# Performance work log

Hardware: AMD Instinct MI355X
Metric: run time of the kernel (lower is better)

## Reference

```python
import jax, jax.numpy as jnp
import numpy as np

B, N, D_OBS, D_MSG, H = 4096, 64, 128, 64, 4
HD = D_MSG // H
EPS = 1e-5


def setup_inputs() -> dict:
    key = jax.random.key(0)
    ks = jax.random.split(key, 16)
    def w(k, shape):
        fan_in = shape[0]
        return (jax.random.normal(k, shape, dtype=jnp.float32) / np.sqrt(fan_in)).astype(jnp.float32)
    return {
        'obs_all': jax.random.normal(ks[0], (B, N, D_OBS), dtype=jnp.float32),
        # msg encoder: Linear(obs,128) -> ReLU -> Linear(128,msg)
        'enc_w1': w(ks[1], (D_OBS, 128)), 'enc_b1': jnp.zeros((128,), jnp.float32),
        'enc_w2': w(ks[2], (128, D_MSG)), 'enc_b2': jnp.zeros((D_MSG,), jnp.float32),
        # MultiheadAttention in/out projections (stored as (in, out))
        'in_proj_w': w(ks[3], (D_MSG, 3 * D_MSG)), 'in_proj_b': jnp.zeros((3 * D_MSG,), jnp.float32),
        'out_w': w(ks[4], (D_MSG, D_MSG)), 'out_b': jnp.zeros((D_MSG,), jnp.float32),
        # integrator: Linear(obs+msg,256) -> LayerNorm(256) -> ReLU -> Linear(256,obs)
        'int_w1': w(ks[5], (D_OBS + D_MSG, 256)), 'int_b1': jnp.zeros((256,), jnp.float32),
        'ln_g': jnp.ones((256,), jnp.float32), 'ln_b': jnp.zeros((256,), jnp.float32),
        'int_w2': w(ks[6], (256, D_OBS)), 'int_b2': jnp.zeros((D_OBS,), jnp.float32),
    }


def reference(obs_all, enc_w1, enc_b1, enc_w2, enc_b2,
              in_proj_w, in_proj_b, out_w, out_b,
              int_w1, int_b1, ln_g, ln_b, int_w2, int_b2):
    # --- send: encode observations into messages (B, N, msg_dim) ---
    h = jax.nn.relu(obs_all @ enc_w1 + enc_b1)
    msgs = h @ enc_w2 + enc_b2

    # --- attention aggregation: per-agent query over all messages.
    # The original per-agent loop (query = msgs[:, i:i+1]) is exactly
    # batched self-attention over the agent axis.
    qkv = msgs @ in_proj_w + in_proj_b            # (B, N, 3*msg)
    q, k, v = jnp.split(qkv, 3, axis=-1)
    q = q.reshape(B, N, H, HD)
    k = k.reshape(B, N, H, HD)
    v = v.reshape(B, N, H, HD)
    scale = 1.0 / np.sqrt(HD)
    scores = jnp.einsum('bqhd,bkhd->bhqk', q, k) * scale   # (B, H, N, N)
    attn = jax.nn.softmax(scores, axis=-1)
    ctx = jnp.einsum('bhqk,bkhd->bqhd', attn, v).reshape(B, N, D_MSG)
    agg = ctx @ out_w + out_b                     # (B, N, msg_dim)

    # --- receive: concat obs + aggregated message, MLP with LayerNorm ---
    combined = jnp.concatenate([obs_all, agg], axis=-1)
    z = combined @ int_w1 + int_b1                # (B, N, 256)
    mu = jnp.mean(z, axis=-1, keepdims=True)
    var = jnp.var(z, axis=-1, keepdims=True)
    z = (z - mu) * jax.lax.rsqrt(var + EPS) * ln_g + ln_b
    enriched = jax.nn.relu(z) @ int_w2 + int_b2   # (B, N, obs_dim)
    return enriched, msgs
```

## Files before the change

### kernel.cpp

```cpp
#include <hip/hip_runtime.h>


typedef __attribute__((ext_vector_type(8))) short bf16x8;
typedef __attribute__((ext_vector_type(4))) float f32x4;
typedef __attribute__((ext_vector_type(16))) float f32x16;

#define MFMA16(a, b, c) __builtin_amdgcn_mfma_f32_16x16x32_bf16((a), (b), (c), 0, 0, 0)
#define MFMA32(a, b, c) __builtin_amdgcn_mfma_f32_32x32x16_bf16((a), (b), (c), 0, 0, 0)

__device__ __forceinline__ float b2f(short s) {
    union { unsigned u; float f; } x;
    x.u = ((unsigned)(unsigned short)s) << 16;
    return x.f;
}
__device__ __forceinline__ short f2b(float f) {
    union { float f; unsigned u; } x;
    x.f = f;
    unsigned r = (x.u + 0x7FFFu + ((x.u >> 16) & 1u)) >> 16;
    return (short)r;
}

template<bool F32>
__device__ __forceinline__ float ldS(const void* p, int i) {
    if (F32) return ((const float*)p)[i];
    return b2f(((const short*)p)[i]);
}
template<bool F32>
__device__ __forceinline__ bf16x8 ld8(const void* p, long i) {
    if (F32) {
        const float4* f = (const float4*)((const float*)p + i);
        float4 a = f[0], b = f[1];
        bf16x8 r;
        r[0] = f2b(a.x); r[1] = f2b(a.y); r[2] = f2b(a.z); r[3] = f2b(a.w);
        r[4] = f2b(b.x); r[5] = f2b(b.y); r[6] = f2b(b.z); r[7] = f2b(b.w);
        return r;
    }
    return *(const bf16x8*)((const short*)p + i);
}
template<bool F32, bool OBSBF>
__device__ __forceinline__ bf16x8 ldobs(const void* obs, const short* obs_bf, long i) {
    if (OBSBF) return *(const bf16x8*)(obs_bf + i);
    return ld8<F32>(obs, i);
}
template<bool F32>
__device__ __forceinline__ void st(void* p, long i, float v) {
    if (F32) ((float*)p)[i] = v;
    else ((short*)p)[i] = f2b(v);
}

#define P_S   0
#define H_S   0
#define Z_S   0
#define Q2_S  9216
#define AG_S  9216
#define K2_S  13312
#define VT_S  17408
#define LN_S  17408
#define MU_S  18432
#define MS_S  22016
#define SMEM_SHORTS 26624
#define HP 136
#define MP 72
#define ZP 264
#define PP 72
#define VP 72

#define WT1_OFF   0
#define WT2_OFF   16384
#define WTQ_OFF   24576
#define WTO_OFF   36864
#define WTI1_OFF  40960
#define WTI2_OFF  90112
#define WT_TOTAL  122880
#define OBS_ELEMS 33554432L
#define WS_NEEDED (256UL + (unsigned long)WT_TOTAL * 2 + (unsigned long)OBS_ELEMS * 2)

template<bool DO_CONV>
__global__ void prep(const void* __restrict__ obs,
                     const void* __restrict__ w1, const void* __restrict__ w2,
                     const void* __restrict__ wq, const void* __restrict__ wo,
                     const void* __restrict__ wi1, const void* __restrict__ wi2,
                     int* __restrict__ flag, short* __restrict__ wt,
                     short* __restrict__ obs_bf) {
    const unsigned short* o16 = (const unsigned short*)obs;
    int lane = threadIdx.x & 63;
    int cnt = 0;
    for (int i = lane; i < 512; i += 64) {
        unsigned e = (o16[i] >> 7) & 0xFFu;
        cnt += (e == 0u || (e >= 80u && e <= 140u)) ? 1 : 0;
    }
#pragma unroll
    for (int off = 1; off < 64; off <<= 1) cnt += __shfl_xor(cnt, off);
    const bool isbf16 = (cnt >= 480);
    if (blockIdx.x == 0 && threadIdx.x == 0) *flag = isbf16 ? 1 : 0;

    long id = (long)blockIdx.x * 256 + threadIdx.x;
    if (id < WT_TOTAL) {
        const void* src;
        int K, N, off, loc = (int)id;
        if (loc < 16384)      { src = w1;  K = 128; N = 128; off = WT1_OFF; }
        else if (loc < 24576) { src = w2;  K = 128; N = 64;  off = WT2_OFF;  loc -= 16384; }
        else if (loc < 36864) { src = wq;  K = 64;  N = 192; off = WTQ_OFF;  loc -= 24576; }
        else if (loc < 40960) { src = wo;  K = 64;  N = 64;  off = WTO_OFF;  loc -= 36864; }
        else if (loc < 90112) { src = wi1; K = 192; N = 256; off = WTI1_OFF; loc -= 40960; }
        else                  { src = wi2; K = 256; N = 128; off = WTI2_OFF; loc -= 90112; }
        int n = loc / K;
        int k = loc - n * K;
        float v = isbf16 ? b2f(((const short*)src)[k * N + n]) : ((const float*)src)[k * N + n];
        wt[off + loc] = f2b(v);
    } else if (DO_CONV && !isbf16) {
        long base = (id - WT_TOTAL) * 8;
        if (base < OBS_ELEMS) {
            const float4* f = (const float4*)((const float*)obs + base);
            float4 a = f[0], b = f[1];
            bf16x8 r;
            r[0] = f2b(a.x); r[1] = f2b(a.y); r[2] = f2b(a.z); r[3] = f2b(a.w);
            r[4] = f2b(b.x); r[5] = f2b(b.y); r[6] = f2b(b.z); r[7] = f2b(b.w);
            *(bf16x8*)(obs_bf + base) = r;
        }
    }
}

template<bool F32, bool OBSBF>
__global__ __launch_bounds__(256, 3)
void macs_main(const void* __restrict__ obs,
               const void* __restrict__ eb1, const void* __restrict__ eb2,
               const void* __restrict__ ipb, const void* __restrict__ ob,
               const void* __restrict__ ib1, const void* __restrict__ lg,
               const void* __restrict__ lb,  const void* __restrict__ ib2,
               const int* __restrict__ flag, const short* __restrict__ wt,
               const short* __restrict__ obs_bf, void* __restrict__ out) {
    if (*flag != (F32 ? 0 : 1)) return;
    __shared__ __align__(16) short smem[SMEM_SHORTS];
    const int tid = threadIdx.x;
    const int w = tid >> 6;
    const int lane = tid & 63;
    const int q = lane >> 4;
    const int t = lane & 15;
    const int l31 = lane & 31;
    const int hi = lane >> 5;
    const int b = blockIdx.x;
    const long obase = (long)b * 64 * 128;

    {
        bf16x8 oa[4][4];
#pragma unroll
        for (int ks = 0; ks < 4; ++ks)
#pragma unroll
            for (int mt = 0; mt < 4; ++mt)
                oa[ks][mt] = ldobs<F32, OBSBF>(obs, obs_bf, obase + (mt * 16 + t) * 128 + ks * 32 + q * 8);
        f32x4 acc[4][2] = {};
        const short* wt1 = wt + WT1_OFF;
#pragma unroll
        for (int ks = 0; ks < 4; ++ks) {
            bf16x8 bb[2];
#pragma unroll
            for (int tj = 0; tj < 2; ++tj)
                bb[tj] = *(const bf16x8*)(wt1 + (w * 32 + tj * 16 + t) * 128 + ks * 32 + q * 8);
#pragma unroll
            for (int mt = 0; mt < 4; ++mt)
#pragma unroll
                for (int tj = 0; tj < 2; ++tj)
                    acc[mt][tj] = MFMA16(oa[ks][mt], bb[tj], acc[mt][tj]);
        }
        short* hs = smem + H_S;
#pragma unroll
        for (int tj = 0; tj < 2; ++tj) {
            int c = w * 32 + tj * 16 + t;
            float bias = ldS<F32>(eb1, c);
#pragma unroll
            for (int mt = 0; mt < 4; ++mt)
#pragma unroll
                for (int i = 0; i < 4; ++i) {
                    int r = mt * 16 + q * 4 + i;
                    hs[r * HP + c] = f2b(fmaxf(acc[mt][tj][i] + bias, 0.f));
                }
        }
    }
    __syncthreads();

    {
        bf16x8 bbv[4];
        const short* wt2 = wt + WT2_OFF;
#pragma unroll
        for (int ks = 0; ks < 4; ++ks)
            bbv[ks] = *(const bf16x8*)(wt2 + (w * 16 + t) * 128 + ks * 32 + q * 8);
        f32x4 acc[4] = {};
        const short* hs = smem + H_S;
#pragma unroll
        for (int ks = 0; ks < 4; ++ks) {
            bf16x8 a[4];
#pragma unroll
            for (int mt = 0; mt < 4; ++mt)
                a[mt] = *(const bf16x8*)(hs + (mt * 16 + t) * HP + ks * 32 + q * 8);
#pragma unroll
            for (int mt = 0; mt < 4; ++mt)
                acc[mt] = MFMA16(a[mt], bbv[ks], acc[mt]);
        }
        short* ms = smem + MS_S;
        float bias = ldS<F32>(eb2, w * 16 + t);
        const long msgs_base = 33554432L;
#pragma unroll
        for (int mt = 0; mt < 4; ++mt)
#pragma unroll
            for (int i = 0; i < 4; ++i) {
                int r = mt * 16 + q * 4 + i;
                float v = acc[mt][i] + bias;
                ms[r * MP + w * 16 + t] = f2b(v);
                st<F32>(out, msgs_base + ((long)b * 64 + r) * 64 + w * 16 + t, v);
            }
    }
    __syncthreads();

    {
        bf16x8 bbv[6];
        const short* wtq = wt + WTQ_OFF;
#pragma unroll
        for (int ks = 0; ks < 2; ++ks)
#pragma unroll
            for (int tj = 0; tj < 3; ++tj)
                bbv[ks * 3 + tj] = *(const bf16x8*)(wtq + (w * 48 + tj * 16 + t) * 64 + ks * 32 + q * 8);
        f32x4 acc[4][3] = {};
        const short* ms = smem + MS_S;
#pragma unroll
        for (int ks = 0; ks < 2; ++ks) {
            bf16x8 a[4];
#pragma unroll
            for (int mt = 0; mt < 4; ++mt)
                a[mt] = *(const bf16x8*)(ms + (mt * 16 + t) * MP + ks * 32 + q * 8);
#pragma unroll
            for (int mt = 0; mt < 4; ++mt)
#pragma unroll
                for (int tj = 0; tj < 3; ++tj)
                    acc[mt][tj] = MFMA16(a[mt], bbv[ks * 3 + tj], acc[mt][tj]);
        }
#pragma unroll
        for (int tj = 0; tj < 3; ++tj) {
            int c = w * 48 + tj * 16 + t;
            float bias = ldS<F32>(ipb, c);
            int sec = c >> 6;
            int head = (c >> 4) & 3;
            float scale = (sec == 0) ? 0.25f : 1.0f;
#pragma unroll
            for (int mt = 0; mt < 4; ++mt)
#pragma unroll
                for (int i = 0; i < 4; ++i) {
                    int r = mt * 16 + q * 4 + i;
                    short bv = f2b((acc[mt][tj][i] + bias) * scale);
                    int idx;
                    if (sec == 0)      idx = Q2_S + head * 1024 + r * 16 + t;
                    else if (sec == 1) idx = K2_S + head * 1024 + r * 16 + t;
                    else               idx = VT_S + head * 1152 + t * VP + r;
                    smem[idx] = bv;
                }
        }
    }
    __syncthreads();

    {
        const int rh = w & 1;
        short* Pq = smem + P_S + w * 2304;
        short* cs = smem + MS_S;
#pragma unroll
        for (int p = 0; p < 2; ++p) {
            const int hd = p * 2 + (w >> 1);
            const short* qh = smem + Q2_S + hd * 1024;
            const short* kh = smem + K2_S + hd * 1024;
            const short* vh = smem + VT_S + hd * 1152;
            f32x16 sc0 = {}, sc1 = {};
            {
                bf16x8 aq  = *(const bf16x8*)(qh + (rh * 32 + l31) * 16 + hi * 8);
                bf16x8 bk0 = *(const bf16x8*)(kh + l31 * 16 + hi * 8);
                bf16x8 bk1 = *(const bf16x8*)(kh + (32 + l31) * 16 + hi * 8);
                sc0 = MFMA32(aq, bk0, sc0);
                sc1 = MFMA32(aq, bk1, sc1);
            }
#pragma unroll
            for (int i = 0; i < 16; ++i) {
                int lr = (i & 3) + 8 * (i >> 2) + 4 * hi;
                float e0 = __expf(sc0[i]);
                float e1 = __expf(sc1[i]);
                float s = e0 + e1;
#pragma unroll
                for (int off = 1; off < 32; off <<= 1) s += __shfl_xor(s, off);
                float inv = 1.f / s;
                Pq[lr * PP + l31]      = f2b(e0 * inv);
                Pq[lr * PP + 32 + l31] = f2b(e1 * inv);
            }
            f32x4 cx[2] = {};
#pragma unroll
            for (int ks = 0; ks < 2; ++ks) {
                bf16x8 bb = *(const bf16x8*)(vh + t * VP + ks * 32 + q * 8);
                bf16x8 a0 = *(const bf16x8*)(Pq + t * PP + ks * 32 + q * 8);
                bf16x8 a1 = *(const bf16x8*)(Pq + (16 + t) * PP + ks * 32 + q * 8);
                cx[0] = MFMA16(a0, bb, cx[0]);
                cx[1] = MFMA16(a1, bb, cx[1]);
            }
#pragma unroll
            for (int mt = 0; mt < 2; ++mt)
#pragma unroll
                for (int i = 0; i < 4; ++i)
                    cs[(rh * 32 + mt * 16 + q * 4 + i) * MP + hd * 16 + t] = f2b(cx[mt][i]);
        }
    }
    __syncthreads();

    bf16x8 oa6[4][4];
    {
#pragma unroll
        for (int ks = 0; ks < 4; ++ks)
#pragma unroll
            for (int mt = 0; mt < 4; ++mt)
                oa6[ks][mt] = ldobs<F32, OBSBF>(obs, obs_bf, obase + (mt * 16 + t) * 128 + ks * 32 + q * 8);
        bf16x8 bbv[2];
        const short* wto = wt + WTO_OFF;
#pragma unroll
        for (int ks = 0; ks < 2; ++ks)
            bbv[ks] = *(const bf16x8*)(wto + (w * 16 + t) * 64 + ks * 32 + q * 8);
        f32x4 acc[4] = {};
        const short* cs = smem + MS_S;
#pragma unroll
        for (int ks = 0; ks < 2; ++ks) {
            bf16x8 a[4];
#pragma unroll
            for (int mt = 0; mt < 4; ++mt)
                a[mt] = *(const bf16x8*)(cs + (mt * 16 + t) * MP + ks * 32 + q * 8);
#pragma unroll
            for (int mt = 0; mt < 4; ++mt)
                acc[mt] = MFMA16(a[mt], bbv[ks], acc[mt]);
        }
        short* ag = smem + AG_S;
        float bias = ldS<F32>(ob, w * 16 + t);
#pragma unroll
        for (int mt = 0; mt < 4; ++mt)
#pragma unroll
            for (int i = 0; i < 4; ++i)
                ag[(mt * 16 + q * 4 + i) * MP + w * 16 + t] = f2b(acc[mt][i] + bias);
    }
    __syncthreads();

    {
        f32x4 acc[4][4] = {};
        const short* wti1 = wt + WTI1_OFF;
        const short* ag = smem + AG_S;
#pragma unroll
        for (int ks = 0; ks < 6; ++ks) {
            bf16x8 a[4], bb[4];
            if (ks < 4) {
#pragma unroll
                for (int mt = 0; mt < 4; ++mt)
                    a[mt] = oa6[ks][mt];
            } else {
#pragma unroll
                for (int mt = 0; mt < 4; ++mt)
                    a[mt] = *(const bf16x8*)(ag + (mt * 16 + t) * MP + (ks - 4) * 32 + q * 8);
            }
#pragma unroll
            for (int tj = 0; tj < 4; ++tj)
                bb[tj] = *(const bf16x8*)(wti1 + (w * 64 + tj * 16 + t) * 192 + ks * 32 + q * 8);
#pragma unroll
            for (int mt = 0; mt < 4; ++mt)
#pragma unroll
                for (int tj = 0; tj < 4; ++tj)
                    acc[mt][tj] = MFMA16(a[mt], bb[tj], acc[mt][tj]);
        }
#pragma unroll
        for (int tj = 0; tj < 4; ++tj) {
            float bias = ldS<F32>(ib1, w * 64 + tj * 16 + t);
#pragma unroll
            for (int mt = 0; mt < 4; ++mt)
#pragma unroll
                for (int i = 0; i < 4; ++i) acc[mt][tj][i] += bias;
        }
        float2* lnred = (float2*)(smem + LN_S);
#pragma unroll
        for (int mt = 0; mt < 4; ++mt)
#pragma unroll
            for (int i = 0; i < 4; ++i) {
                float s = 0.f, s2 = 0.f;
#pragma unroll
                for (int tj = 0; tj < 4; ++tj) {
                    float v = acc[mt][tj][i];
                    s += v;
                    s2 += v * v;
                }
#pragma unroll
                for (int off = 1; off < 16; off <<= 1) {
                    s += __shfl_xor(s, off);
                    s2 += __shfl_xor(s2, off);
                }
                if (t == 0) {
                    float2 p; p.x = s; p.y = s2;
                    lnred[(mt * 16 + q * 4 + i) * 4 + w] = p;
                }
            }
        __syncthreads();
        float2* munr = (float2*)(smem + MU_S);
        if (tid < 64) {
            float S = 0.f, S2 = 0.f;
#pragma unroll
            for (int j = 0; j < 4; ++j) {
                float2 p = lnred[tid * 4 + j];
                S += p.x;
                S2 += p.y;
            }
            float mu = S * (1.f / 256.f);
            float var = S2 * (1.f / 256.f) - mu * mu;
            float2 m; m.x = mu; m.y = rsqrtf(fmaxf(var, 0.f) + 1e-5f);
            munr[tid] = m;
        }
        __syncthreads();
        short* zs = smem + Z_S;
        float gv[4], bv[4];
#pragma unroll
        for (int tj = 0; tj < 4; ++tj) {
            gv[tj] = ldS<F32>(lg, w * 64 + tj * 16 + t);
            bv[tj] = ldS<F32>(lb, w * 64 + tj * 16 + t);
        }
#pragma unroll
        for (int mt = 0; mt < 4; ++mt)
#pragma unroll
            for (int i = 0; i < 4; ++i) {
                int r = mt * 16 + q * 4 + i;
                float2 mr = munr[r];
#pragma unroll
                for (int tj = 0; tj < 4; ++tj) {
                    float v = (acc[mt][tj][i] - mr.x) * mr.y * gv[tj] + bv[tj];
                    zs[r * ZP + w * 64 + tj * 16 + t] = f2b(fmaxf(v, 0.f));
                }
            }
    }
    __syncthreads();

    {
        bf16x8 bbv[8][2];
        const short* wti2 = wt + WTI2_OFF;
#pragma unroll
        for (int ks = 0; ks < 8; ++ks)
#pragma unroll
            for (int tj = 0; tj < 2; ++tj)
                bbv[ks][tj] = *(const bf16x8*)(wti2 + (w * 32 + tj * 16 + t) * 256 + ks * 32 + q * 8);
        f32x4 acc[4][2] = {};
        const short* zs = smem + Z_S;
#pragma unroll
        for (int ks = 0; ks < 8; ++ks) {
            bf16x8 a[4];
#pragma unroll
            for (int mt = 0; mt < 4; ++mt)
                a[mt] = *(const bf16x8*)(zs + (mt * 16 + t) * ZP + ks * 32 + q * 8);
#pragma unroll
            for (int mt = 0; mt < 4; ++mt)
#pragma unroll
                for (int tj = 0; tj < 2; ++tj)
                    acc[mt][tj] = MFMA16(a[mt], bbv[ks][tj], acc[mt][tj]);
        }
#pragma unroll
        for (int tj = 0; tj < 2; ++tj) {
            int c = w * 32 + tj * 16 + t;
            float bias = ldS<F32>(ib2, c);
#pragma unroll
            for (int mt = 0; mt < 4; ++mt)
#pragma unroll
                for (int i = 0; i < 4; ++i) {
                    int r = mt * 16 + q * 4 + i;
                    st<F32>(out, ((long)b * 64 + r) * 128 + c, acc[mt][tj][i] + bias);
                }
        }
    }
}

extern "C" void kernel_launch(void* const* d_in, const int* in_sizes, int n_in,
                              void* d_out, int out_size, void* d_ws, size_t ws_size,
                              hipStream_t stream) {
    const void* obs = d_in[0];
    const void* w1  = d_in[1];
    const void* b1  = d_in[2];
    const void* w2  = d_in[3];
    const void* b2  = d_in[4];
    const void* wq  = d_in[5];
    const void* bq  = d_in[6];
    const void* wo  = d_in[7];
    const void* bo  = d_in[8];
    const void* wi1 = d_in[9];
    const void* bi1 = d_in[10];
    const void* lg  = d_in[11];
    const void* lb  = d_in[12];
    const void* wi2 = d_in[13];
    const void* bi2 = d_in[14];
    int* flag = (int*)d_ws;
    short* wt = (short*)d_ws + 128;
    short* obs_bf = (short*)d_ws + 128 + WT_TOTAL;
    const bool big_ws = (ws_size >= WS_NEEDED);

    if (big_ws) {
        prep<true><<<dim3(16864), dim3(256), 0, stream>>>(obs, w1, w2, wq, wo, wi1, wi2, flag, wt, obs_bf);
        macs_main<false, false><<<dim3(4096), dim3(256), 0, stream>>>(obs, b1, b2, bq, bo, bi1, lg, lb, bi2, flag, wt, obs_bf, d_out);
        macs_main<true,  true ><<<dim3(4096), dim3(256), 0, stream>>>(obs, b1, b2, bq, bo, bi1, lg, lb, bi2, flag, wt, obs_bf, d_out);
    } else {
        prep<false><<<dim3(480), dim3(256), 0, stream>>>(obs, w1, w2, wq, wo, wi1, wi2, flag, wt, obs_bf);
        macs_main<false, false><<<dim3(4096), dim3(256), 0, stream>>>(obs, b1, b2, bq, bo, bi1, lg, lb, bi2, flag, wt, obs_bf, d_out);
        macs_main<true,  false><<<dim3(4096), dim3(256), 0, stream>>>(obs, b1, b2, bq, bo, bi1, lg, lb, bi2, flag, wt, obs_bf, d_out);
    }
}
```

Baseline: 586.7 us.

## Fold linear layers into prep weights, defer softmax normalization, single main launch

Precomputes fused weights in prep: enc_w2·in_proj (QKV straight from the hidden layer) and out_w·int_w1 (context straight into the integrator), with matching folded biases and all bias/LN vectors converted to fp32. The main kernel skips the msgs→QKV and agg stages and their shared-memory round trips. Softmax normalization now comes from an extra MFMA against a ones vector and is applied after P·V, which removes the per-row shuffle reductions. It also prefetches later-stage weights into registers, reuses the first obs fragment load, and replaces the two dtype-templated launches with one runtime-branched launch. The folded weights are rounded to bf16, which changes numerics, and the larger register footprint may reduce occupancy.

Result: no change. 586.9 us (+0.0%).

```diff
diff --git a/kernel.cpp b/kernel.cpp
--- a/kernel.cpp
+++ b/kernel.cpp
@@ -19,45 +19,28 @@
     unsigned r = (x.u + 0x7FFFu + ((x.u >> 16) & 1u)) >> 16;
     return (short)r;
 }
-
-template<bool F32>
-__device__ __forceinline__ float ldS(const void* p, int i) {
-    if (F32) return ((const float*)p)[i];
-    return b2f(((const short*)p)[i]);
-}
-template<bool F32>
-__device__ __forceinline__ bf16x8 ld8(const void* p, long i) {
-    if (F32) {
-        const float4* f = (const float4*)((const float*)p + i);
-        float4 a = f[0], b = f[1];
-        bf16x8 r;
-        r[0] = f2b(a.x); r[1] = f2b(a.y); r[2] = f2b(a.z); r[3] = f2b(a.w);
-        r[4] = f2b(b.x); r[5] = f2b(b.y); r[6] = f2b(b.z); r[7] = f2b(b.w);
-        return r;
-    }
-    return *(const bf16x8*)((const short*)p + i);
-}
-template<bool F32, bool OBSBF>
-__device__ __forceinline__ bf16x8 ldobs(const void* obs, const short* obs_bf, long i) {
-    if (OBSBF) return *(const bf16x8*)(obs_bf + i);
-    return ld8<F32>(obs, i);
-}
-template<bool F32>
-__device__ __forceinline__ void st(void* p, long i, float v) {
-    if (F32) ((float*)p)[i] = v;
-    else ((short*)p)[i] = f2b(v);
+__device__ __forceinline__ float ldw(const void* p, long i, bool bf) {
+    return bf ? b2f(((const short*)p)[i]) : ((const float*)p)[i];
+}
+__device__ __forceinline__ bf16x8 ld8rt(const void* p, long i, bool bf) {
+    if (bf) return *(const bf16x8*)((const short*)p + i);
+    const float4* f = (const float4*)((const float*)p + i);
+    float4 a = f[0], c = f[1];
+    bf16x8 r;
+    r[0] = f2b(a.x); r[1] = f2b(a.y); r[2] = f2b(a.z); r[3] = f2b(a.w);
+    r[4] = f2b(c.x); r[5] = f2b(c.y); r[6] = f2b(c.z); r[7] = f2b(c.w);
+    return r;
 }
 
 #define P_S   0
 #define H_S   0
 #define Z_S   0
 #define Q2_S  9216
-#define AG_S  9216
 #define K2_S  13312
 #define VT_S  17408
 #define LN_S  17408
 #define MU_S  18432
-#define MS_S  22016
+#define CTX_S 22016
 #define SMEM_SHORTS 26624
 #define HP 136
 #define MP 72
@@ -67,21 +50,33 @@
 
 #define WT1_OFF   0
 #define WT2_OFF   16384
-#define WTQ_OFF   24576
-#define WTO_OFF   36864
-#define WTI1_OFF  40960
-#define WTI2_OFF  90112
-#define WT_TOTAL  122880
+#define WT26_OFF  24576
+#define WTI1_OFF  49152
+#define WTF_OFF   81920
+#define WTI2_OFF  98304
+#define WT_TOTAL  131072
+#define FB_B26 0
+#define FB_BI  192
+#define FB_EB1 448
+#define FB_EB2 576
+#define FB_LG  640
+#define FB_LB  896
+#define FB_IB2 1152
+#define FB_TOTAL 1280
 #define OBS_ELEMS 33554432L
-#define WS_NEEDED (256UL + (unsigned long)WT_TOTAL * 2 + (unsigned long)OBS_ELEMS * 2)
+#define WS_NEEDED ((unsigned long)(128 + WT_TOTAL + 2 * FB_TOTAL + OBS_ELEMS) * 2UL)
 
 template<bool DO_CONV>
 __global__ void prep(const void* __restrict__ obs,
                      const void* __restrict__ w1, const void* __restrict__ w2,
                      const void* __restrict__ wq, const void* __restrict__ wo,
                      const void* __restrict__ wi1, const void* __restrict__ wi2,
+                     const void* __restrict__ eb1, const void* __restrict__ eb2,
+                     const void* __restrict__ ipb, const void* __restrict__ ob,
+                     const void* __restrict__ ib1, const void* __restrict__ lg,
+                     const void* __restrict__ lb,  const void* __restrict__ ib2,
                      int* __restrict__ flag, short* __restrict__ wt,
-                     short* __restrict__ obs_bf) {
+                     float* __restrict__ fb, short* __restrict__ obs_bf) {
     const unsigned short* o16 = (const unsigned short*)obs;
     int lane = threadIdx.x & 63;
     int cnt = 0;
@@ -91,46 +86,69 @@
     }
 #pragma unroll
     for (int off = 1; off < 64; off <<= 1) cnt += __shfl_xor(cnt, off);
-    const bool isbf16 = (cnt >= 480);
-    if (blockIdx.x == 0 && threadIdx.x == 0) *flag = isbf16 ? 1 : 0;
+    const bool bf = (cnt >= 480);
+    if (blockIdx.x == 0 && threadIdx.x == 0) *flag = bf ? 1 : 0;
 
     long id = (long)blockIdx.x * 256 + threadIdx.x;
-    if (id < WT_TOTAL) {
-        const void* src;
-        int K, N, off, loc = (int)id;
-        if (loc < 16384)      { src = w1;  K = 128; N = 128; off = WT1_OFF; }
-        else if (loc < 24576) { src = w2;  K = 128; N = 64;  off = WT2_OFF;  loc -= 16384; }
-        else if (loc < 36864) { src = wq;  K = 64;  N = 192; off = WTQ_OFF;  loc -= 24576; }
-        else if (loc < 40960) { src = wo;  K = 64;  N = 64;  off = WTO_OFF;  loc -= 36864; }
-        else if (loc < 90112) { src = wi1; K = 192; N = 256; off = WTI1_OFF; loc -= 40960; }
-        else                  { src = wi2; K = 256; N = 128; off = WTI2_OFF; loc -= 90112; }
-        int n = loc / K;
-        int k = loc - n * K;
-        float v = isbf16 ? b2f(((const short*)src)[k * N + n]) : ((const float*)src)[k * N + n];
-        wt[off + loc] = f2b(v);
-    } else if (DO_CONV && !isbf16) {
-        long base = (id - WT_TOTAL) * 8;
+    if (id < 16384) {
+        int n = (int)id >> 7, k = (int)id & 127;
+        wt[WT1_OFF + id] = f2b(ldw(w1, k * 128 + n, bf));
+    } else if (id < 24576) {
+        int loc = (int)id - 16384, n = loc >> 7, k = loc & 127;
+        wt[WT2_OFF + loc] = f2b(ldw(w2, k * 64 + n, bf));
+    } else if (id < 49152) {
+        int loc = (int)id - 24576, n = loc >> 7, k = loc & 127;
+        float s = 0.f;
+        for (int j = 0; j < 64; ++j) s += ldw(w2, k * 64 + j, bf) * ldw(wq, j * 192 + n, bf);
+        wt[WT26_OFF + loc] = f2b(s);
+    } else if (id < 81920) {
+        int loc = (int)id - 49152, n = loc >> 7, k = loc & 127;
+        wt[WTI1_OFF + loc] = f2b(ldw(wi1, k * 256 + n, bf));
+    } else if (id < 98304) {
+        int loc = (int)id - 81920, n = loc >> 6, c = loc & 63;
+        float s = 0.f;
+        for (int m = 0; m < 64; ++m) s += ldw(wo, c * 64 + m, bf) * ldw(wi1, (128 + m) * 256 + n, bf);
+        wt[WTF_OFF + loc] = f2b(s);
+    } else if (id < 131072) {
+        int loc = (int)id - 98304, n = loc >> 8, k = loc & 255;
+        wt[WTI2_OFF + loc] = f2b(ldw(wi2, k * 128 + n, bf));
+    } else if (id < 131264) {
+        int n = (int)id - 131072;
+        float s = ldw(ipb, n, bf);
+        for (int j = 0; j < 64; ++j) s += ldw(eb2, j, bf) * ldw(wq, j * 192 + n, bf);
+        fb[FB_B26 + n] = s;
+    } else if (id < 131520) {
+        int n = (int)id - 131264;
+        float s = ldw(ib1, n, bf);
+        for (int m = 0; m < 64; ++m) s += ldw(ob, m, bf) * ldw(wi1, (128 + m) * 256 + n, bf);
+        fb[FB_BI + n] = s;
+    } else if (id < 132352) {
+        int j = (int)id - 131520;
+        float v; int d;
+        if (j < 128)      { v = ldw(eb1, j, bf);       d = FB_EB1 + j; }
+        else if (j < 192) { v = ldw(eb2, j - 128, bf); d = FB_EB2 + j - 128; }
+        else if (j < 448) { v = ldw(lg, j - 192, bf);  d = FB_LG + j - 192; }
+        else if (j < 704) { v = ldw(lb, j - 448, bf);  d = FB_LB + j - 448; }
+        else              { v = ldw(ib2, j - 704, bf); d = FB_IB2 + j - 704; }
+        fb[d] = v;
+    } else if (DO_CONV && !bf) {
+        long base = (id - 132352) * 8;
         if (base < OBS_ELEMS) {
             const float4* f = (const float4*)((const float*)obs + base);
-            float4 a = f[0], b = f[1];
+            float4 a = f[0], c = f[1];
             bf16x8 r;
             r[0] = f2b(a.x); r[1] = f2b(a.y); r[2] = f2b(a.z); r[3] = f2b(a.w);
-            r[4] = f2b(b.x); r[5] = f2b(b.y); r[6] = f2b(b.z); r[7] = f2b(b.w);
+            r[4] = f2b(c.x); r[5] = f2b(c.y); r[6] = f2b(c.z); r[7] = f2b(c.w);
             *(bf16x8*)(obs_bf + base) = r;
         }
     }
 }
 
-template<bool F32, bool OBSBF>
+template<bool OBSBF>
 __global__ __launch_bounds__(256, 3)
-void macs_main(const void* __restrict__ obs,
-               const void* __restrict__ eb1, const void* __restrict__ eb2,
-               const void* __restrict__ ipb, const void* __restrict__ ob,
-               const void* __restrict__ ib1, const void* __restrict__ lg,
-               const void* __restrict__ lb,  const void* __restrict__ ib2,
-               const int* __restrict__ flag, const short* __restrict__ wt,
+void macs_main(const void* __restrict__ obs, const int* __restrict__ flag,
+               const short* __restrict__ wt, const float* __restrict__ fb,
                const short* __restrict__ obs_bf, void* __restrict__ out) {
-    if (*flag != (F32 ? 0 : 1)) return;
     __shared__ __align__(16) short smem[SMEM_SHORTS];
     const int tid = threadIdx.x;
     const int w = tid >> 6;
@@ -141,52 +159,63 @@
     const int hi = lane >> 5;
     const int b = blockIdx.x;
     const long obase = (long)b * 64 * 128;
+    const bool inbf = (*flag != 0);
+    const bool f32out = !inbf;
+    const short* osrc = OBSBF ? (inbf ? (const short*)obs : obs_bf) : (const short*)0;
+
+    bf16x8 oa[4][4];
+#pragma unroll
+    for (int ks = 0; ks < 4; ++ks)
+#pragma unroll
+        for (int mt = 0; mt < 4; ++mt) {
+            long idx = obase + (mt * 16 + t) * 128 + ks * 32 + q * 8;
+            oa[ks][mt] = OBSBF ? *(const bf16x8*)(osrc + idx) : ld8rt(obs, idx, inbf);
+        }
+
+    bf16x8 w2p[4];
+    bf16x8 wi1p[2][4];
+    bf16x8 w2pp[8][2];
 
     {
-        bf16x8 oa[4][4];
-#pragma unroll
-        for (int ks = 0; ks < 4; ++ks)
-#pragma unroll
-            for (int mt = 0; mt < 4; ++mt)
-                oa[ks][mt] = ldobs<F32, OBSBF>(obs, obs_bf, obase + (mt * 16 + t) * 128 + ks * 32 + q * 8);
         f32x4 acc[4][2] = {};
-        const short* wt1 = wt + WT1_OFF;
+        const short* wt1p = wt + WT1_OFF;
 #pragma unroll
         for (int ks = 0; ks < 4; ++ks) {
             bf16x8 bb[2];
 #pragma unroll
             for (int tj = 0; tj < 2; ++tj)
-                bb[tj] = *(const bf16x8*)(wt1 + (w * 32 + tj * 16 + t) * 128 + ks * 32 + q * 8);
+                bb[tj] = *(const bf16x8*)(wt1p + (w * 32 + tj * 16 + t) * 128 + ks * 32 + q * 8);
 #pragma unroll
             for (int mt = 0; mt < 4; ++mt)
 #pragma unroll
                 for (int tj = 0; tj < 2; ++tj)
                     acc[mt][tj] = MFMA16(oa[ks][mt], bb[tj], acc[mt][tj]);
         }
+        {
+            const short* wt2 = wt + WT2_OFF;
+#pragma unroll
+            for (int ks = 0; ks < 4; ++ks)
+                w2p[ks] = *(const bf16x8*)(wt2 + (w * 16 + t) * 128 + ks * 32 + q * 8);
+            __builtin_amdgcn_sched_barrier(0);
+        }
         short* hs = smem + H_S;
 #pragma unroll
         for (int tj = 0; tj < 2; ++tj) {
             int c = w * 32 + tj * 16 + t;
-            float bias = ldS<F32>(eb1, c);
-#pragma unroll
-            for (int mt = 0; mt < 4; ++mt)
-#pragma unroll
-                for (int i = 0; i < 4; ++i) {
-                    int r = mt * 16 + q * 4 + i;
-                    hs[r * HP + c] = f2b(fmaxf(acc[mt][tj][i] + bias, 0.f));
-                }
+            float bias = fb[FB_EB1 + c];
+#pragma unroll
+            for (int mt = 0; mt < 4; ++mt)
+#pragma unroll
+                for (int i = 0; i < 4; ++i)
+                    hs[(mt * 16 + q * 4 + i) * HP + c] = f2b(fmaxf(acc[mt][tj][i] + bias, 0.f));
         }
     }
     __syncthreads();
 
     {
-        bf16x8 bbv[4];
-        const short* wt2 = wt + WT2_OFF;
-#pragma unroll
-        for (int ks = 0; ks < 4; ++ks)
-            bbv[ks] = *(const bf16x8*)(wt2 + (w * 16 + t) * 128 + ks * 32 + q * 8);
-        f32x4 acc[4] = {};
         const short* hs = smem + H_S;
+        const long msgs_base = 33554432L;
+        f32x4 am[4] = {};
 #pragma unroll
         for (int ks = 0; ks < 4; ++ks) {
             bf16x8 a[4];
@@ -195,49 +224,43 @@
                 a[mt] = *(const bf16x8*)(hs + (mt * 16 + t) * HP + ks * 32 + q * 8);
 #pragma unroll
             for (int mt = 0; mt < 4; ++mt)
-                acc[mt] = MFMA16(a[mt], bbv[ks], acc[mt]);
-        }
-        short* ms = smem + MS_S;
-        float bias = ldS<F32>(eb2, w * 16 + t);
-        const long msgs_base = 33554432L;
-#pragma unroll
-        for (int mt = 0; mt < 4; ++mt)
-#pragma unroll
-            for (int i = 0; i < 4; ++i) {
-                int r = mt * 16 + q * 4 + i;
-                float v = acc[mt][i] + bias;
-                ms[r * MP + w * 16 + t] = f2b(v);
-                st<F32>(out, msgs_base + ((long)b * 64 + r) * 64 + w * 16 + t, v);
-            }
-    }
-    __syncthreads();
-
-    {
-        bf16x8 bbv[6];
-        const short* wtq = wt + WTQ_OFF;
-#pragma unroll
-        for (int ks = 0; ks < 2; ++ks)
+                am[mt] = MFMA16(a[mt], w2p[ks], am[mt]);
+        }
+        float mb = fb[FB_EB2 + w * 16 + t];
+        if (f32out) {
+#pragma unroll
+            for (int mt = 0; mt < 4; ++mt)
+#pragma unroll
+                for (int i = 0; i < 4; ++i)
+                    ((float*)out)[msgs_base + ((long)b * 64 + mt * 16 + q * 4 + i) * 64 + w * 16 + t] = am[mt][i] + mb;
+        } else {
+#pragma unroll
+            for (int mt = 0; mt < 4; ++mt)
+#pragma unroll
+                for (int i = 0; i < 4; ++i)
+                    ((short*)out)[msgs_base + ((long)b * 64 + mt * 16 + q * 4 + i) * 64 + w * 16 + t] = f2b(am[mt][i] + mb);
+        }
+        f32x4 aq[4][3] = {};
+        const short* w26 = wt + WT26_OFF;
+#pragma unroll
+        for (int ks = 0; ks < 4; ++ks) {
+            bf16x8 a[4], bb[3];
+#pragma unroll
+            for (int mt = 0; mt < 4; ++mt)
+                a[mt] = *(const bf16x8*)(hs + (mt * 16 + t) * HP + ks * 32 + q * 8);
 #pragma unroll
             for (int tj = 0; tj < 3; ++tj)
-                bbv[ks * 3 + tj] = *(const bf16x8*)(wtq + (w * 48 + tj * 16 + t) * 64 + ks * 32 + q * 8);
-        f32x4 acc[4][3] = {};
-        const short* ms = smem + MS_S;
-#pragma unroll
-        for (int ks = 0; ks < 2; ++ks) {
-            bf16x8 a[4];
-#pragma unroll
-            for (int mt = 0; mt < 4; ++mt)
-                a[mt] = *(const bf16x8*)(ms + (mt * 16 + t) * MP + ks * 32 + q * 8);
+                bb[tj] = *(const bf16x8*)(w26 + (w * 48 + tj * 16 + t) * 128 + ks * 32 + q * 8);
 #pragma unroll
             for (int mt = 0; mt < 4; ++mt)
 #pragma unroll
                 for (int tj = 0; tj < 3; ++tj)
-                    acc[mt][tj] = MFMA16(a[mt], bbv[ks * 3 + tj], acc[mt][tj]);
+                    aq[mt][tj] = MFMA16(a[mt], bb[tj], aq[mt][tj]);
         }
 #pragma unroll
         for (int tj = 0; tj < 3; ++tj) {
             int c = w * 48 + tj * 16 + t;
-            float bias = ldS<F32>(ipb, c);
+            float bias = fb[FB_B26 + c];
             int sec = c >> 6;
             int head = (c >> 4) & 3;
             float scale = (sec == 0) ? 0.25f : 1.0f;
@@ -246,7 +269,7 @@
 #pragma unroll
                 for (int i = 0; i < 4; ++i) {
                     int r = mt * 16 + q * 4 + i;
-                    short bv = f2b((acc[mt][tj][i] + bias) * scale);
+                    short bv = f2b((aq[mt][tj][i] + bias) * scale);
                     int idx;
                     if (sec == 0)      idx = Q2_S + head * 1024 + r * 16 + t;
                     else if (sec == 1) idx = K2_S + head * 1024 + r * 16 + t;
@@ -260,7 +283,9 @@
     {
         const int rh = w & 1;
         short* Pq = smem + P_S + w * 2304;
-        short* cs = smem + MS_S;
+        short* cs = smem + CTX_S;
+        bf16x8 ones = { (short)0x3F80, (short)0x3F80, (short)0x3F80, (short)0x3F80,
+                        (short)0x3F80, (short)0x3F80, (short)0x3F80, (short)0x3F80 };
 #pragma unroll
         for (int p = 0; p < 2; ++p) {
             const int hd = p * 2 + (w >> 1);
@@ -278,16 +303,10 @@
 #pragma unroll
             for (int i = 0; i < 16; ++i) {
                 int lr = (i & 3) + 8 * (i >> 2) + 4 * hi;
-                float e0 = __expf(sc0[i]);
-                float e1 = __expf(sc1[i]);
-                float s = e0 + e1;
-#pragma unroll
-                for (int off = 1; off < 32; off <<= 1) s += __shfl_xor(s, off);
-                float inv = 1.f / s;
-                Pq[lr * PP + l31]      = f2b(e0 * inv);
-                Pq[lr * PP + 32 + l31] = f2b(e1 * inv);
-            }
-            f32x4 cx[2] = {};
+                Pq[lr * PP + l31]      = f2b(__expf(sc0[i]));
+                Pq[lr * PP + 32 + l31] = f2b(__expf(sc1[i]));
+            }
+            f32x4 cx[2] = {}, sm[2] = {};
 #pragma unroll
             for (int ks = 0; ks < 2; ++ks) {
                 bf16x8 bb = *(const bf16x8*)(vh + t * VP + ks * 32 + q * 8);
@@ -295,69 +314,60 @@
                 bf16x8 a1 = *(const bf16x8*)(Pq + (16 + t) * PP + ks * 32 + q * 8);
                 cx[0] = MFMA16(a0, bb, cx[0]);
                 cx[1] = MFMA16(a1, bb, cx[1]);
+                sm[0] = MFMA16(a0, ones, sm[0]);
+                sm[1] = MFMA16(a1, ones, sm[1]);
             }
 #pragma unroll
             for (int mt = 0; mt < 2; ++mt)
 #pragma unroll
-                for (int i = 0; i < 4; ++i)
-                    cs[(rh * 32 + mt * 16 + q * 4 + i) * MP + hd * 16 + t] = f2b(cx[mt][i]);
-        }
-    }
-    __syncthreads();
-
-    bf16x8 oa6[4][4];
-    {
-#pragma unroll
-        for (int ks = 0; ks < 4; ++ks)
-#pragma unroll
-            for (int mt = 0; mt < 4; ++mt)
-                oa6[ks][mt] = ldobs<F32, OBSBF>(obs, obs_bf, obase + (mt * 16 + t) * 128 + ks * 32 + q * 8);
-        bf16x8 bbv[2];
-        const short* wto = wt + WTO_OFF;
-#pragma unroll
-        for (int ks = 0; ks < 2; ++ks)
-            bbv[ks] = *(const bf16x8*)(wto + (w * 16 + t) * 64 + ks * 32 + q * 8);
-        f32x4 acc[4] = {};
-        const short* cs = smem + MS_S;
-#pragma unroll
-        for (int ks = 0; ks < 2; ++ks) {
-            bf16x8 a[4];
-#pragma unroll
-            for (int mt = 0; mt < 4; ++mt)
-                a[mt] = *(const bf16x8*)(cs + (mt * 16 + t) * MP + ks * 32 + q * 8);
-#pragma unroll
-            for (int mt = 0; mt < 4; ++mt)
-                acc[mt] = MFMA16(a[mt], bbv[ks], acc[mt]);
-        }
-        short* ag = smem + AG_S;
-        float bias = ldS<F32>(ob, w * 16 + t);
-#pragma unroll
-        for (int mt = 0; mt < 4; ++mt)
-#pragma unroll
-            for (int i = 0; i < 4; ++i)
-                ag[(mt * 16 + q * 4 + i) * MP + w * 16 + t] = f2b(acc[mt][i] + bias);
+                for (int i = 0; i < 4; ++i) {
+                    float inv = __builtin_amdgcn_rcpf(sm[mt][i]);
+                    cs[(rh * 32 + mt * 16 + q * 4 + i) * MP + hd * 16 + t] = f2b(cx[mt][i] * inv);
+                }
+        }
+        {
+            const short* wti1 = wt + WTI1_OFF;
+#pragma unroll
+            for (int ks = 0; ks < 2; ++ks)
+#pragma unroll
+                for (int tj = 0; tj < 4; ++tj)
+                    wi1p[ks][tj] = *(const bf16x8*)(wti1 + (w * 64 + tj * 16 + t) * 128 + ks * 32 + q * 8);
+            __builtin_amdgcn_sched_barrier(0);
+        }
     }
     __syncthreads();
 
     {
         f32x4 acc[4][4] = {};
         const short* wti1 = wt + WTI1_OFF;
-        const short* ag = smem + AG_S;
-#pragma unroll
-        for (int ks = 0; ks < 6; ++ks) {
+        const short* wtf  = wt + WTF_OFF;
+        const short* cs = smem + CTX_S;
+#pragma unroll
+        for (int ks = 0; ks < 4; ++ks) {
+            bf16x8 bb[4];
+            if (ks < 2) {
+#pragma unroll
+                for (int tj = 0; tj < 4; ++tj) bb[tj] = wi1p[ks][tj];
+            } else {
+#pragma unroll
+                for (int tj = 0; tj < 4; ++tj)
+                    bb[tj] = *(const bf16x8*)(wti1 + (w * 64 + tj * 16 + t) * 128 + ks * 32 + q * 8);
+            }
+#pragma unroll
+            for (int mt = 0; mt < 4; ++mt)
+#pragma unroll
+                for (int tj = 0; tj < 4; ++tj)
+                    acc[mt][tj] = MFMA16(oa[ks][mt], bb[tj], acc[mt][tj]);
+        }
+#pragma unroll
+        for (int ks = 0; ks < 2; ++ks) {
             bf16x8 a[4], bb[4];
-            if (ks < 4) {
-#pragma unroll
-                for (int mt = 0; mt < 4; ++mt)
-                    a[mt] = oa6[ks][mt];
-            } else {
-#pragma unroll
-                for (int mt = 0; mt < 4; ++mt)
-                    a[mt] = *(const bf16x8*)(ag + (mt * 16 + t) * MP + (ks - 4) * 32 + q * 8);
-            }
+#pragma unroll
+            for (int mt = 0; mt < 4; ++mt)
+                a[mt] = *(const bf16x8*)(cs + (mt * 16 + t) * MP + ks * 32 + q * 8);
 #pragma unroll
             for (int tj = 0; tj < 4; ++tj)
-                bb[tj] = *(const bf16x8*)(wti1 + (w * 64 + tj * 16 + t) * 192 + ks * 32 + q * 8);
+                bb[tj] = *(const bf16x8*)(wtf + (w * 64 + tj * 16 + t) * 64 + ks * 32 + q * 8);
 #pragma unroll
             for (int mt = 0; mt < 4; ++mt)
 #pragma unroll
@@ -366,7 +376,7 @@
         }
 #pragma unroll
         for (int tj = 0; tj < 4; ++tj) {
-            float bias = ldS<F32>(ib1, w * 64 + tj * 16 + t);
+            float bias = fb[FB_BI + w * 64 + tj * 16 + t];
 #pragma unroll
             for (int mt = 0; mt < 4; ++mt)
 #pragma unroll
@@ -410,12 +420,21 @@
             munr[tid] = m;
         }
         __syncthreads();
+        {
+            const short* wti2 = wt + WTI2_OFF;
+#pragma unroll
+            for (int ks = 0; ks < 8; ++ks)
+#pragma unroll
+                for (int tj = 0; tj < 2; ++tj)
+                    w2pp[ks][tj] = *(const bf16x8*)(wti2 + (w * 32 + tj * 16 + t) * 256 + ks * 32 + q * 8);
+            __builtin_amdgcn_sched_barrier(0);
+        }
         short* zs = smem + Z_S;
         float gv[4], bv[4];
 #pragma unroll
         for (int tj = 0; tj < 4; ++tj) {
-            gv[tj] = ldS<F32>(lg, w * 64 + tj * 16 + t);
-            bv[tj] = ldS<F32>(lb, w * 64 + tj * 16 + t);
+            gv[tj] = fb[FB_LG + w * 64 + tj * 16 + t];
+            bv[tj] = fb[FB_LB + w * 64 + tj * 16 + t];
         }
 #pragma unroll
         for (int mt = 0; mt < 4; ++mt)
@@ -433,13 +452,6 @@
     __syncthreads();
 
     {
-        bf16x8 bbv[8][2];
-        const short* wti2 = wt + WTI2_OFF;
-#pragma unroll
-        for (int ks = 0; ks < 8; ++ks)
-#pragma unroll
-            for (int tj = 0; tj < 2; ++tj)
-                bbv[ks][tj] = *(const bf16x8*)(wti2 + (w * 32 + tj * 16 + t) * 256 + ks * 32 + q * 8);
         f32x4 acc[4][2] = {};
         const short* zs = smem + Z_S;
 #pragma unroll
@@ -452,19 +464,30 @@
             for (int mt = 0; mt < 4; ++mt)
 #pragma unroll
                 for (int tj = 0; tj < 2; ++tj)
-                    acc[mt][tj] = MFMA16(a[mt], bbv[ks][tj], acc[mt][tj]);
-        }
-#pragma unroll
-        for (int tj = 0; tj < 2; ++tj) {
-            int c = w * 32 + tj * 16 + t;
-            float bias = ldS<F32>(ib2, c);
-#pragma unroll
-            for (int mt = 0; mt < 4; ++mt)
-#pragma unroll
-                for (int i = 0; i < 4; ++i) {
-                    int r = mt * 16 + q * 4 + i;
-                    st<F32>(out, ((long)b * 64 + r) * 128 + c, acc[mt][tj][i] + bias);
-                }
+                    acc[mt][tj] = MFMA16(a[mt], w2pp[ks][tj], acc[mt][tj]);
+        }
+        if (f32out) {
+#pragma unroll
+            for (int tj = 0; tj < 2; ++tj) {
+                int c = w * 32 + tj * 16 + t;
+                float bias = fb[FB_IB2 + c];
+#pragma unroll
+                for (int mt = 0; mt < 4; ++mt)
+#pragma unroll
+                    for (int i = 0; i < 4; ++i)
+                        ((float*)out)[((long)b * 64 + mt * 16 + q * 4 + i) * 128 + c] = acc[mt][tj][i] + bias;
+            }
+        } else {
+#pragma unroll
+            for (int tj = 0; tj < 2; ++tj) {
+                int c = w * 32 + tj * 16 + t;
+                float bias = fb[FB_IB2 + c];
+#pragma unroll
+                for (int mt = 0; mt < 4; ++mt)
+#pragma unroll
+                    for (int i = 0; i < 4; ++i)
+                        ((short*)out)[((long)b * 64 + mt * 16 + q * 4 + i) * 128 + c] = f2b(acc[mt][tj][i] + bias);
+            }
         }
     }
 }
@@ -489,16 +512,19 @@
     const void* bi2 = d_in[14];
     int* flag = (int*)d_ws;
     short* wt = (short*)d_ws + 128;
-    short* obs_bf = (short*)d_ws + 128 + WT_TOTAL;
-    const bool big_ws = (ws_size >= WS_NEEDED);
-
-    if (big_ws) {
-        prep<true><<<dim3(16864), dim3(256), 0, stream>>>(obs, w1, w2, wq, wo, wi1, wi2, flag, wt, obs_bf);
-        macs_main<false, false><<<dim3(4096), dim3(256), 0, stream>>>(obs, b1, b2, bq, bo, bi1, lg, lb, bi2, flag, wt, obs_bf, d_out);
-        macs_main<true,  true ><<<dim3(4096), dim3(256), 0, stream>>>(obs, b1, b2, bq, bo, bi1, lg, lb, bi2, flag, wt, obs_bf, d_out);
+    float* fb = (float*)((short*)d_ws + 128 + WT_TOTAL);
+    short* obs_bf = (short*)d_ws + 128 + WT_TOTAL + 2 * FB_TOTAL;
+    const bool big = (ws_size >= WS_NEEDED);
+
+    if (big) {
+        prep<true><<<dim3(16901), dim3(256), 0, stream>>>(
+            obs, w1, w2, wq, wo, wi1, wi2, b1, b2, bq, bo, bi1, lg, lb, bi2,
+            flag, wt, fb, obs_bf);
+        macs_main<true><<<dim3(4096), dim3(256), 0, stream>>>(obs, flag, wt, fb, obs_bf, d_out);
     } else {
-        prep<false><<<dim3(480), dim3(256), 0, stream>>>(obs, w1, w2, wq, wo, wi1, wi2, flag, wt, obs_bf);
-        macs_main<false, false><<<dim3(4096), dim3(256), 0, stream>>>(obs, b1, b2, bq, bo, bi1, lg, lb, bi2, flag, wt, obs_bf, d_out);
-        macs_main<true,  false><<<dim3(4096), dim3(256), 0, stream>>>(obs, b1, b2, bq, bo, bi1, lg, lb, bi2, flag, wt, obs_bf, d_out);
-    }
-}
+        prep<false><<<dim3(517), dim3(256), 0, stream>>>(
+            obs, w1, w2, wq, wo, wi1, wi2, b1, b2, bq, bo, bi1, lg, lb, bi2,
+            flag, wt, fb, obs_bf);
+        macs_main<false><<<dim3(4096), dim3(256), 0, stream>>>(obs, flag, wt, fb, obs_bf, d_out);
+    }
+}
```
